# Optimization experiments

Hardware: AMD Instinct MI355X
Metric: run time of the kernel (lower is better)

## Reference

```python
import jax, jax.numpy as jnp
import numpy as np

N_NODES = 50000
D_IN = 64
HID = 64
OUT = 64
NEG_SLOPE = 0.2


def setup_inputs() -> dict:
    key = jax.random.key(0)
    ks = jax.random.split(key, 16)
    s = 1.0 / np.sqrt(D_IN)
    inp = {
        "x": jax.random.normal(ks[0], (N_NODES, D_IN), dtype=jnp.float32),
        "edge_index": jax.random.randint(ks[1], (2, 1200000), 0, N_NODES, dtype=jnp.int64),
        # conv1 (GATConv, heads=1): separate src/dst projections + attention vectors + bias
        "W1_src": jax.random.uniform(ks[2], (D_IN, HID), jnp.float32, -s, s),
        "W1_dst": jax.random.uniform(ks[3], (D_IN, HID), jnp.float32, -s, s),
        "att1_src": jax.random.uniform(ks[4], (HID,), jnp.float32, -s, s),
        "att1_dst": jax.random.uniform(ks[5], (HID,), jnp.float32, -s, s),
        "b1": jnp.zeros((HID,), jnp.float32),
        # lin1 residual
        "Wl1": jax.random.uniform(ks[6], (D_IN, HID), jnp.float32, -s, s),
        "bl1": jnp.zeros((HID,), jnp.float32),
        # conv2
        "W2_src": jax.random.uniform(ks[7], (HID, OUT), jnp.float32, -s, s),
        "W2_dst": jax.random.uniform(ks[8], (HID, OUT), jnp.float32, -s, s),
        "att2_src": jax.random.uniform(ks[9], (OUT,), jnp.float32, -s, s),
        "att2_dst": jax.random.uniform(ks[10], (OUT,), jnp.float32, -s, s),
        "b2": jnp.zeros((OUT,), jnp.float32),
        # lin2 residual
        "Wl2": jax.random.uniform(ks[11], (HID, OUT), jnp.float32, -s, s),
        "bl2": jnp.zeros((OUT,), jnp.float32),
    }
    return inp


def _gat_conv(x, W_src, W_dst, att_src, att_dst, bias, src, dst, n_nodes):
    # project nodes: [N, C]
    h_src = x @ W_src
    h_dst = x @ W_dst
    # per-node attention logits: [N]
    a_src = h_src @ att_src
    a_dst = h_dst @ att_dst
    # per-edge score, leaky relu (slope 0.2)
    e = a_src[src] + a_dst[dst]  # [E]
    e = jnp.where(e >= 0, e, NEG_SLOPE * e)
    # segment softmax over incoming edges of each dst node
    seg_max = jax.lax.stop_gradient(
        jax.ops.segment_max(e, dst, num_segments=n_nodes))  # [N]
    w = jnp.exp(e - seg_max[dst])  # [E]
    seg_sum = jax.ops.segment_sum(w, dst, num_segments=n_nodes)  # [N]
    alpha = w / seg_sum[dst]  # [E]
    # weighted scatter-add of gathered src features
    msg = h_src[src] * alpha[:, None]  # [E, C]
    out = jax.ops.segment_sum(msg, dst, num_segments=n_nodes)  # [N, C]
    return out + bias


def reference(x, edge_index, W1_src, W1_dst, att1_src, att1_dst, b1, Wl1, bl1,
              W2_src, W2_dst, att2_src, att2_dst, b2, Wl2, bl2):
    src, dst = edge_index[0], edge_index[1]
    n = x.shape[0]
    h = _gat_conv(x, W1_src, W1_dst, att1_src, att1_dst, b1, src, dst, n)
    h = jax.nn.relu(h + x @ Wl1 + bl1)
    o = _gat_conv(h, W2_src, W2_dst, att2_src, att2_dst, b2, src, dst, n)
    o = jax.nn.relu(o + h @ Wl2 + bl2)
    return o
```

## Files before the change

### kernel.cpp

```cpp
#include <hip/hip_runtime.h>
#include <hip/hip_fp16.h>

#define NEG 0.2f
#define BSHIFT 9
#define BNODES 512
#define ECAP 14336

__device__ __forceinline__ void agg_core(
    int beg, int end, float ad, int lane, int g, int l,
    const int* __restrict__ ssrc, const float* __restrict__ asrc,
    const float2* __restrict__ h8,
    float& a0, float& a1, float& a2, float& a3, float& sumw) {
    a0 = a1 = a2 = a3 = sumw = 0.f;
    while (beg < end) {
        int nb = min(64, end - beg);
        int s_l = 0; float w_l = 0.f;
        if (lane < nb) {
            s_l = ssrc[beg + lane];
            float e = asrc[s_l] + ad;
            e = (e >= 0.f) ? e : NEG * e;
            w_l = __expf(e);
        }
        int i = 0;
        for (; i + 7 < nb; i += 8) {
            int iA = i + g, iB = i + 4 + g;
            int   sA = __shfl(s_l, iA, 64), sB = __shfl(s_l, iB, 64);
            float wA = __shfl(w_l, iA, 64), wB = __shfl(w_l, iB, 64);
            float2 rA = h8[(size_t)sA * 16 + l];
            float2 rB = h8[(size_t)sB * 16 + l];
            float2 fA0 = __half22float2(((const __half2*)&rA)[0]);
            float2 fA1 = __half22float2(((const __half2*)&rA)[1]);
            float2 fB0 = __half22float2(((const __half2*)&rB)[0]);
            float2 fB1 = __half22float2(((const __half2*)&rB)[1]);
            sumw += wA + wB;
            a0 += wA * fA0.x + wB * fB0.x;
            a1 += wA * fA0.y + wB * fB0.y;
            a2 += wA * fA1.x + wB * fB1.x;
            a3 += wA * fA1.y + wB * fB1.y;
        }
        for (; i < nb; i += 4) {
            int iA = i + g;
            int   sA = __shfl(s_l, iA, 64);
            float wA = __shfl(w_l, iA, 64);
            float2 rA = h8[(size_t)sA * 16 + l];
            float2 fA0 = __half22float2(((const __half2*)&rA)[0]);
            float2 fA1 = __half22float2(((const __half2*)&rA)[1]);
            sumw += wA;
            a0 += wA * fA0.x; a1 += wA * fA0.y;
            a2 += wA * fA1.x; a3 += wA * fA1.y;
        }
        beg += nb;
    }
    a0 += __shfl_xor(a0, 16, 64); a0 += __shfl_xor(a0, 32, 64);
    a1 += __shfl_xor(a1, 16, 64); a1 += __shfl_xor(a1, 32, 64);
    a2 += __shfl_xor(a2, 16, 64); a2 += __shfl_xor(a2, 32, 64);
    a3 += __shfl_xor(a3, 16, 64); a3 += __shfl_xor(a3, 32, 64);
    sumw += __shfl_xor(sumw, 16, 64); sumw += __shfl_xor(sumw, 32, 64);
}

__global__ __launch_bounds__(256) void bin_prep(
    const int* __restrict__ src, const int* __restrict__ dst,
    int* __restrict__ gcur, unsigned* __restrict__ binned, int E, int K,
    const float* __restrict__ W1s, const float* __restrict__ a1s,
    const float* __restrict__ W1d, const float* __restrict__ a1d,
    const float* __restrict__ W2s, const float* __restrict__ a2s,
    const float* __restrict__ W2d, const float* __restrict__ a2d,
    float* __restrict__ vecs) {
    int t = threadIdx.x;
    if (blockIdx.x == gridDim.x - 1) {
        int g = t >> 6, k = t & 63;
        const float* W = (g == 0) ? W1s : (g == 1) ? W1d : (g == 2) ? W2s : W2d;
        const float* a = (g == 0) ? a1s : (g == 1) ? a1d : (g == 2) ? a2s : a2d;
        float s = 0.f;
        #pragma unroll 8
        for (int j = 0; j < 64; ++j) s += W[k * 64 + j] * a[j];
        vecs[t] = s;
        return;
    }
    __shared__ int h[128], cbase[128], cur[128];
    if (t < 128) h[t] = 0;
    __syncthreads();
    int base = blockIdx.x * 2048;
    #pragma unroll
    for (int i = 0; i < 8; ++i) {
        int idx = base + i * 256 + t;
        if (idx < E) atomicAdd(&h[dst[idx] >> BSHIFT], 1);
    }
    __syncthreads();
    if (t < K) {
        cbase[t] = t * ECAP + (h[t] ? atomicAdd(&gcur[t], h[t]) : 0);
        cur[t] = 0;
    }
    __syncthreads();
    #pragma unroll
    for (int i = 0; i < 8; ++i) {
        int idx = base + i * 256 + t;
        if (idx < E) {
            int d = dst[idx], s = src[idx];
            int b = d >> BSHIFT;
            int pos = cbase[b] + atomicAdd(&cur[b], 1);
            binned[pos] = ((unsigned)s << BSHIFT) | (unsigned)(d & (BNODES - 1));
        }
    }
}

__device__ __forceinline__ void gemm_tile(
    int tid, int row0, int rows,
    const __half* WsH, const __half* WlH, const float* xs,
    const float* bias_s, const float* vs_s, const float* vd_s,
    __half2* __restrict__ hsrc, float* __restrict__ base_out,
    float* __restrict__ asrc, float* __restrict__ adst) {
    int r0 = (tid >> 3) * 2;
    int cg = tid & 7, c0 = cg * 8;
    if (r0 >= rows) return;

    float a0[8], a1[8], b0[8], b1[8];
    #pragma unroll
    for (int i = 0; i < 8; ++i) { a0[i] = a1[i] = b0[i] = b1[i] = 0.f; }
    float as0 = 0.f, ad0 = 0.f, as1 = 0.f, ad1 = 0.f;

    #pragma unroll 8
    for (int k = 0; k < 64; ++k) {
        float xv0 = xs[r0 * 65 + k];
        float xv1 = xs[(r0 + 1) * 65 + k];
        float4 wsv = *(const float4*)&WsH[(k << 6) + c0];
        float4 wlv = *(const float4*)&WlH[(k << 6) + c0];
        const __half2* hs = (const __half2*)&wsv;
        const __half2* hl = (const __half2*)&wlv;
        #pragma unroll
        for (int p = 0; p < 4; ++p) {
            float2 w = __half22float2(hs[p]);
            a0[2*p]   += xv0 * w.x;  a0[2*p+1] += xv0 * w.y;
            a1[2*p]   += xv1 * w.x;  a1[2*p+1] += xv1 * w.y;
            float2 l = __half22float2(hl[p]);
            b0[2*p]   += xv0 * l.x;  b0[2*p+1] += xv0 * l.y;
            b1[2*p]   += xv1 * l.x;  b1[2*p+1] += xv1 * l.y;
        }
        float vsk = vs_s[k], vdk = vd_s[k];
        as0 += xv0 * vsk;  ad0 += xv0 * vdk;
        as1 += xv1 * vsk;  ad1 += xv1 * vdk;
    }

    int rg0 = row0 + r0, rg1 = rg0 + 1;
    bool row1ok = (r0 + 1) < rows;
    float4 pack;
    ((__half2*)&pack)[0] = __floats2half2_rn(a0[0], a0[1]);
    ((__half2*)&pack)[1] = __floats2half2_rn(a0[2], a0[3]);
    ((__half2*)&pack)[2] = __floats2half2_rn(a0[4], a0[5]);
    ((__half2*)&pack)[3] = __floats2half2_rn(a0[6], a0[7]);
    *(float4*)&hsrc[(size_t)rg0 * 32 + (c0 >> 1)] = pack;
    if (row1ok) {
        ((__half2*)&pack)[0] = __floats2half2_rn(a1[0], a1[1]);
        ((__half2*)&pack)[1] = __floats2half2_rn(a1[2], a1[3]);
        ((__half2*)&pack)[2] = __floats2half2_rn(a1[4], a1[5]);
        ((__half2*)&pack)[3] = __floats2half2_rn(a1[6], a1[7]);
        *(float4*)&hsrc[(size_t)rg1 * 32 + (c0 >> 1)] = pack;
    }
    float4 bA = *(const float4*)&bias_s[c0];
    float4 bB = *(const float4*)&bias_s[c0 + 4];
    float4 o;
    o.x = b0[0] + bA.x; o.y = b0[1] + bA.y; o.z = b0[2] + bA.z; o.w = b0[3] + bA.w;
    *(float4*)&base_out[(size_t)rg0 * 64 + c0] = o;
    o.x = b0[4] + bB.x; o.y = b0[5] + bB.y; o.z = b0[6] + bB.z; o.w = b0[7] + bB.w;
    *(float4*)&base_out[(size_t)rg0 * 64 + c0 + 4] = o;
    if (row1ok) {
        o.x = b1[0] + bA.x; o.y = b1[1] + bA.y; o.z = b1[2] + bA.z; o.w = b1[3] + bA.w;
        *(float4*)&base_out[(size_t)rg1 * 64 + c0] = o;
        o.x = b1[4] + bB.x; o.y = b1[5] + bB.y; o.z = b1[6] + bB.z; o.w = b1[7] + bB.w;
        *(float4*)&base_out[(size_t)rg1 * 64 + c0 + 4] = o;
    }
    if (cg == 0) {
        asrc[rg0] = as0; adst[rg0] = ad0;
        if (row1ok) { asrc[rg1] = as1; adst[rg1] = ad1; }
    }
}

__global__ __launch_bounds__(256) void csr_gemm(
    const unsigned* __restrict__ binned, int* __restrict__ ssrc,
    const int* __restrict__ gcur, int* __restrict__ rowbeg, int* __restrict__ rowend,
    const float* __restrict__ x, const float* __restrict__ Wsrc,
    const float* __restrict__ Wl, const float* __restrict__ vsrc,
    const float* __restrict__ vdst, const float* __restrict__ bconv,
    const float* __restrict__ blin,
    __half2* __restrict__ hsrc, float* __restrict__ base_out,
    float* __restrict__ asrc, float* __restrict__ adst, int N, int K) {
    __shared__ union {
        struct { __half WsH[4096]; __half WlH[4096]; float xs[64 * 65];
                 float bias[64]; float vs[64]; float vd[64]; } g;
        struct { int lh[BNODES]; int ps[256]; } c;
    } sm;
    int tid = threadIdx.x;
    int blk = blockIdx.x;

    if (blk < K) {
        int base = blk * ECAP;
        int cnt = min(gcur[blk], ECAP);
        sm.c.lh[tid] = 0; sm.c.lh[tid + 256] = 0;
        __syncthreads();
        for (int i = tid; i < cnt; i += 256)
            atomicAdd(&sm.c.lh[binned[base + i] & (BNODES - 1)], 1);
        __syncthreads();
        int a0 = sm.c.lh[2 * tid], a1 = sm.c.lh[2 * tid + 1];
        sm.c.ps[tid] = a0 + a1;
        __syncthreads();
        for (int off = 1; off < 256; off <<= 1) {
            int v = (tid >= off) ? sm.c.ps[tid - off] : 0;
            __syncthreads();
            sm.c.ps[tid] += v;
            __syncthreads();
        }
        int exc = sm.c.ps[tid] - (a0 + a1);
        int node0 = blk * BNODES + 2 * tid, node1 = node0 + 1;
        if (node0 < N) { rowbeg[node0] = base + exc;      rowend[node0] = base + exc + a0; }
        if (node1 < N) { rowbeg[node1] = base + exc + a0; rowend[node1] = base + exc + a0 + a1; }
        __syncthreads();
        sm.c.lh[2 * tid] = exc; sm.c.lh[2 * tid + 1] = exc + a0;
        __syncthreads();
        for (int i = tid; i < cnt; i += 256) {
            unsigned e = binned[base + i];
            int pos = atomicAdd(&sm.c.lh[e & (BNODES - 1)], 1);
            ssrc[base + pos] = (int)(e >> BSHIFT);
        }
        return;
    }

    int gb = blk - K;
    #pragma unroll
    for (int i = 0; i < 4; ++i) {
        int idx4 = tid * 4 + i * 1024;
        float4 ws = *(const float4*)&Wsrc[idx4];
        float4 wl = *(const float4*)&Wl[idx4];
        *(__half2*)&sm.g.WsH[idx4]     = __floats2half2_rn(ws.x, ws.y);
        *(__half2*)&sm.g.WsH[idx4 + 2] = __floats2half2_rn(ws.z, ws.w);
        *(__half2*)&sm.g.WlH[idx4]     = __floats2half2_rn(wl.x, wl.y);
        *(__half2*)&sm.g.WlH[idx4 + 2] = __floats2half2_rn(wl.z, wl.w);
    }
    if (tid < 64) {
        sm.g.bias[tid] = bconv[tid] + blin[tid];
        sm.g.vs[tid]   = vsrc[tid];
        sm.g.vd[tid]   = vdst[tid];
    }
    int row0 = gb * 64;
    int rows = min(64, N - row0);
    #pragma unroll
    for (int i = 0; i < 16; ++i) {
        int idx = tid + i * 256;
        int r = idx >> 6, cc = idx & 63;
        if (r < rows) sm.g.xs[r * 65 + cc] = x[(size_t)(row0 + r) * 64 + cc];
    }
    __syncthreads();
    gemm_tile(tid, row0, rows, sm.g.WsH, sm.g.WlH, sm.g.xs,
              sm.g.bias, sm.g.vs, sm.g.vd, hsrc, base_out, asrc, adst);
}

__global__ __launch_bounds__(256) void agg_gemm(
    const int* __restrict__ rowbeg, const int* __restrict__ rowend,
    const int* __restrict__ ssrc,
    const float* __restrict__ asrc1, const float* __restrict__ adst1,
    const float2* __restrict__ h8_1, const float* __restrict__ base1,
    const float* __restrict__ Wsrc, const float* __restrict__ Wl,
    const float* __restrict__ vsrc, const float* __restrict__ vdst,
    const float* __restrict__ bconv, const float* __restrict__ blin,
    __half2* __restrict__ hsrc2, float* __restrict__ base2,
    float* __restrict__ asrc2, float* __restrict__ adst2, int N) {
    __shared__ __half WsH[4096];
    __shared__ __half WlH[4096];
    __shared__ float xs[64 * 65];
    __shared__ float bias_s[64], vs_s[64], vd_s[64];

    int tid = threadIdx.x;
    #pragma unroll
    for (int i = 0; i < 4; ++i) {
        int idx4 = tid * 4 + i * 1024;
        float4 ws = *(const float4*)&Wsrc[idx4];
        float4 wl = *(const float4*)&Wl[idx4];
        *(__half2*)&WsH[idx4]     = __floats2half2_rn(ws.x, ws.y);
        *(__half2*)&WsH[idx4 + 2] = __floats2half2_rn(ws.z, ws.w);
        *(__half2*)&WlH[idx4]     = __floats2half2_rn(wl.x, wl.y);
        *(__half2*)&WlH[idx4 + 2] = __floats2half2_rn(wl.z, wl.w);
    }
    if (tid < 64) {
        bias_s[tid] = bconv[tid] + blin[tid];
        vs_s[tid]   = vsrc[tid];
        vd_s[tid]   = vdst[tid];
    }

    int row0 = blockIdx.x * 64;
    int rows = min(64, N - row0);
    int wave = tid >> 6, lane = tid & 63, g = lane >> 4, l = lane & 15;
    #pragma unroll 1
    for (int k = 0; k < 16; ++k) {
        int d = row0 + wave * 16 + k;
        if (d < N) {
            float a0, a1, a2, a3, sw;
            agg_core(rowbeg[d], rowend[d], adst1[d], lane, g, l,
                     ssrc, asrc1, h8_1, a0, a1, a2, a3, sw);
            if (g == 0) {
                float4 b4 = *(const float4*)&base1[(size_t)d * 64 + 4 * l];
                float invw = (sw > 0.f) ? 1.f / sw : 0.f;
                float4 r;
                r.x = fmaxf(b4.x + a0 * invw, 0.f);
                r.y = fmaxf(b4.y + a1 * invw, 0.f);
                r.z = fmaxf(b4.z + a2 * invw, 0.f);
                r.w = fmaxf(b4.w + a3 * invw, 0.f);
                *(float4*)&xs[(d - row0) * 65 + 4 * l] = r;
            }
        }
    }
    __syncthreads();
    gemm_tile(tid, row0, rows, WsH, WlH, xs, bias_s, vs_s, vd_s,
              hsrc2, base2, asrc2, adst2);
}

__global__ __launch_bounds__(256) void gat_aggregate(
    const int* __restrict__ rowbeg, const int* __restrict__ rowend,
    const int* __restrict__ ssrc,
    const float* __restrict__ asrc, const float* __restrict__ adst,
    const float2* __restrict__ h8, const float* __restrict__ base,
    float* __restrict__ out, int N) {
    int d = blockIdx.x * 4 + (threadIdx.x >> 6);
    int lane = threadIdx.x & 63, g = lane >> 4, l = lane & 15;
    if (d >= N) return;
    float a0, a1, a2, a3, sw;
    agg_core(rowbeg[d], rowend[d], adst[d], lane, g, l, ssrc, asrc, h8,
             a0, a1, a2, a3, sw);
    if (g == 0) {
        float4 b4 = *(const float4*)&base[(size_t)d * 64 + 4 * l];
        float invw = (sw > 0.f) ? 1.f / sw : 0.f;
        float4 o;
        o.x = fmaxf(b4.x + a0 * invw, 0.f);
        o.y = fmaxf(b4.y + a1 * invw, 0.f);
        o.z = fmaxf(b4.z + a2 * invw, 0.f);
        o.w = fmaxf(b4.w + a3 * invw, 0.f);
        *(float4*)&out[(size_t)d * 64 + 4 * l] = o;
    }
}

extern "C" void kernel_launch(void* const* d_in, const int* in_sizes, int n_in,
                              void* d_out, int out_size, void* d_ws, size_t ws_size,
                              hipStream_t stream) {
    const float* x    = (const float*)d_in[0];
    const int*   ei   = (const int*)d_in[1];
    const float* W1s  = (const float*)d_in[2];
    const float* W1d  = (const float*)d_in[3];
    const float* a1s  = (const float*)d_in[4];
    const float* a1d  = (const float*)d_in[5];
    const float* b1   = (const float*)d_in[6];
    const float* Wl1  = (const float*)d_in[7];
    const float* bl1  = (const float*)d_in[8];
    const float* W2s  = (const float*)d_in[9];
    const float* W2d  = (const float*)d_in[10];
    const float* a2s  = (const float*)d_in[11];
    const float* a2d  = (const float*)d_in[12];
    const float* b2   = (const float*)d_in[13];
    const float* Wl2  = (const float*)d_in[14];
    const float* bl2  = (const float*)d_in[15];

    const int N = in_sizes[0] / 64;
    const int E = in_sizes[1] / 2;
    const int* src = ei;
    const int* dst = ei + E;
    const int K = (N + BNODES - 1) >> BSHIFT;

    float* ws = (float*)d_ws;
    size_t o = 0;
    __half2* hsrc1 = (__half2*)(ws + o); o += (size_t)N * 32;
    __half2* hsrc2 = (__half2*)(ws + o); o += (size_t)N * 32;
    float* base   = ws + o; o += (size_t)N * 64;
    float* asrc1  = ws + o; o += N;
    float* adst1  = ws + o; o += N;
    float* asrc2  = ws + o; o += N;
    float* adst2  = ws + o; o += N;
    float* vecs   = ws + o; o += 256;
    int* rowbeg = (int*)(ws + o); o += N;
    int* rowend = (int*)(ws + o); o += N;
    int* gcur   = (int*)(ws + o); o += 128;
    unsigned* binned = (unsigned*)(ws + o); o += (size_t)K * ECAP;
    int* ssrc   = (int*)(ws + o); o += (size_t)K * ECAP;

    const int EB = (E + 2047) / 2048;
    const int GB = (N + 63) / 64;

    hipMemsetAsync(gcur, 0, 128 * sizeof(int), stream);
    bin_prep<<<EB + 1, 256, 0, stream>>>(src, dst, gcur, binned, E, K,
                                         W1s, a1s, W1d, a1d, W2s, a2s, W2d, a2d, vecs);

    csr_gemm<<<K + GB, 256, 0, stream>>>(
        binned, ssrc, gcur, rowbeg, rowend,
        x, W1s, Wl1, vecs, vecs + 64, b1, bl1,
        hsrc1, base, asrc1, adst1, N, K);

    agg_gemm<<<GB, 256, 0, stream>>>(
        rowbeg, rowend, ssrc, asrc1, adst1, (const float2*)hsrc1, base,
        W2s, Wl2, vecs + 128, vecs + 192, b2, bl2,
        hsrc2, base, asrc2, adst2, N);

    gat_aggregate<<<(N + 3) / 4, 256, 0, stream>>>(
        rowbeg, rowend, ssrc, asrc2, adst2, (const float2*)hsrc2, base,
        (float*)d_out, N);
}
```

Before: 247.7 us.

## Unfuse layer-2 aggregation from GEMM into separate aggregate and node GEMM kernels

Replaces the fused agg_gemm kernel, in which each block aggregated 64 nodes serially per wave before running the second-layer GEMM, with the existing per-node gat_aggregate kernel writing the intermediate activations to the output buffer, followed by a standalone node_gemm. The aim is more parallelism and better latency hiding in the gather-heavy aggregation, since the fused kernel had few blocks and a long serial per-wave loop. In exchange it adds a kernel launch and a round trip of the hidden layer through global memory. Workspace buffers are reused across layers.

```diff
diff --git a/kernel.cpp b/kernel.cpp
--- a/kernel.cpp
+++ b/kernel.cpp
@@ -253,16 +253,13 @@
               sm.g.bias, sm.g.vs, sm.g.vd, hsrc, base_out, asrc, adst);
 }
 
-__global__ __launch_bounds__(256) void agg_gemm(
-    const int* __restrict__ rowbeg, const int* __restrict__ rowend,
-    const int* __restrict__ ssrc,
-    const float* __restrict__ asrc1, const float* __restrict__ adst1,
-    const float2* __restrict__ h8_1, const float* __restrict__ base1,
-    const float* __restrict__ Wsrc, const float* __restrict__ Wl,
-    const float* __restrict__ vsrc, const float* __restrict__ vdst,
-    const float* __restrict__ bconv, const float* __restrict__ blin,
-    __half2* __restrict__ hsrc2, float* __restrict__ base2,
-    float* __restrict__ asrc2, float* __restrict__ adst2, int N) {
+__global__ __launch_bounds__(256) void node_gemm(
+    const float* __restrict__ x, const float* __restrict__ Wsrc,
+    const float* __restrict__ Wl, const float* __restrict__ vsrc,
+    const float* __restrict__ vdst, const float* __restrict__ bconv,
+    const float* __restrict__ blin,
+    __half2* __restrict__ hsrc, float* __restrict__ base_out,
+    float* __restrict__ asrc, float* __restrict__ adst, int n) {
     __shared__ __half WsH[4096];
     __shared__ __half WlH[4096];
     __shared__ float xs[64 * 65];
@@ -284,32 +281,17 @@
         vs_s[tid]   = vsrc[tid];
         vd_s[tid]   = vdst[tid];
     }
-
     int row0 = blockIdx.x * 64;
-    int rows = min(64, N - row0);
-    int wave = tid >> 6, lane = tid & 63, g = lane >> 4, l = lane & 15;
-    #pragma unroll 1
-    for (int k = 0; k < 16; ++k) {
-        int d = row0 + wave * 16 + k;
-        if (d < N) {
-            float a0, a1, a2, a3, sw;
-            agg_core(rowbeg[d], rowend[d], adst1[d], lane, g, l,
-                     ssrc, asrc1, h8_1, a0, a1, a2, a3, sw);
-            if (g == 0) {
-                float4 b4 = *(const float4*)&base1[(size_t)d * 64 + 4 * l];
-                float invw = (sw > 0.f) ? 1.f / sw : 0.f;
-                float4 r;
-                r.x = fmaxf(b4.x + a0 * invw, 0.f);
-                r.y = fmaxf(b4.y + a1 * invw, 0.f);
-                r.z = fmaxf(b4.z + a2 * invw, 0.f);
-                r.w = fmaxf(b4.w + a3 * invw, 0.f);
-                *(float4*)&xs[(d - row0) * 65 + 4 * l] = r;
-            }
-        }
+    int rows = min(64, n - row0);
+    #pragma unroll
+    for (int i = 0; i < 16; ++i) {
+        int idx = tid + i * 256;
+        int r = idx >> 6, cc = idx & 63;
+        if (r < rows) xs[r * 65 + cc] = x[(size_t)(row0 + r) * 64 + cc];
     }
     __syncthreads();
     gemm_tile(tid, row0, rows, WsH, WlH, xs, bias_s, vs_s, vd_s,
-              hsrc2, base2, asrc2, adst2);
+              hsrc, base_out, asrc, adst);
 }
 
 __global__ __launch_bounds__(256) void gat_aggregate(
@@ -364,13 +346,10 @@
 
     float* ws = (float*)d_ws;
     size_t o = 0;
-    __half2* hsrc1 = (__half2*)(ws + o); o += (size_t)N * 32;
-    __half2* hsrc2 = (__half2*)(ws + o); o += (size_t)N * 32;
+    __half2* hsrcH = (__half2*)(ws + o); o += (size_t)N * 32;
     float* base   = ws + o; o += (size_t)N * 64;
-    float* asrc1  = ws + o; o += N;
-    float* adst1  = ws + o; o += N;
-    float* asrc2  = ws + o; o += N;
-    float* adst2  = ws + o; o += N;
+    float* asrc   = ws + o; o += N;
+    float* adst   = ws + o; o += N;
     float* vecs   = ws + o; o += 256;
     int* rowbeg = (int*)(ws + o); o += N;
     int* rowend = (int*)(ws + o); o += N;
@@ -378,24 +357,27 @@
     unsigned* binned = (unsigned*)(ws + o); o += (size_t)K * ECAP;
     int* ssrc   = (int*)(ws + o); o += (size_t)K * ECAP;
 
+    float* hmid = (float*)d_out;
+
     const int EB = (E + 2047) / 2048;
     const int GB = (N + 63) / 64;
 
-    hipMemsetAsync(gcur, 0, 128 * sizeof(int), stream);
+    (void)hipMemsetAsync(gcur, 0, 128 * sizeof(int), stream);
     bin_prep<<<EB + 1, 256, 0, stream>>>(src, dst, gcur, binned, E, K,
                                          W1s, a1s, W1d, a1d, W2s, a2s, W2d, a2d, vecs);
 
     csr_gemm<<<K + GB, 256, 0, stream>>>(
         binned, ssrc, gcur, rowbeg, rowend,
         x, W1s, Wl1, vecs, vecs + 64, b1, bl1,
-        hsrc1, base, asrc1, adst1, N, K);
-
-    agg_gemm<<<GB, 256, 0, stream>>>(
-        rowbeg, rowend, ssrc, asrc1, adst1, (const float2*)hsrc1, base,
-        W2s, Wl2, vecs + 128, vecs + 192, b2, bl2,
-        hsrc2, base, asrc2, adst2, N);
+        hsrcH, base, asrc, adst, N, K);
 
     gat_aggregate<<<(N + 3) / 4, 256, 0, stream>>>(
-        rowbeg, rowend, ssrc, asrc2, adst2, (const float2*)hsrc2, base,
+        rowbeg, rowend, ssrc, asrc, adst, (const float2*)hsrcH, base, hmid, N);
+
+    node_gemm<<<GB, 256, 0, stream>>>(hmid, W2s, Wl2, vecs + 128, vecs + 192,
+                                      b2, bl2, hsrcH, base, asrc, adst, N);
+
+    gat_aggregate<<<(N + 3) / 4, 256, 0, stream>>>(
+        rowbeg, rowend, ssrc, asrc, adst, (const float2*)hsrcH, base,
         (float*)d_out, N);
 }
```

New measurement: 235.4 us. 1.05x faster.
